# Kernel optimization log

Measured on AMD Instinct MI355X. Metric: run time of the kernel, lower is better.

## Reference

```python
import jax, jax.numpy as jnp
import numpy as np
import math

B, Q, D = 2, 2048, 1024
H, R = 16, 12
DH = D // H
RHO = 2.0
MAX_OFFSET = 6.0


def setup_inputs() -> dict:
    key = jax.random.key(0)
    ks = jax.random.split(key, 16)
    s = 0.02
    inp = {
        'x': jax.random.normal(ks[0], (B, Q, D), dtype=jnp.float32),
        'wq': jax.random.normal(ks[1], (D, D), dtype=jnp.float32) * s,
        'bq': jnp.zeros((D,), jnp.float32),
        'wk': jax.random.normal(ks[2], (D, D), dtype=jnp.float32) * s,
        'bk': jnp.zeros((D,), jnp.float32),
        'wv': jax.random.normal(ks[3], (D, D), dtype=jnp.float32) * s,
        'bv': jnp.zeros((D,), jnp.float32),
        'wo': jax.random.normal(ks[4], (D, D), dtype=jnp.float32) * s,
        'bo': jnp.zeros((D,), jnp.float32),
        'dw_w': jax.random.normal(ks[5], (D, 1, 3), dtype=jnp.float32) * s,  # depthwise conv1d k=3
        'dw_b': jnp.zeros((D,), jnp.float32),
        'pw_w': jax.random.normal(ks[6], (H * R, D), dtype=jnp.float32) * s,  # pointwise conv1d k=1
        'pw_b': jnp.zeros((H * R,), jnp.float32),
        'rel_scale': jnp.asarray(0.1, jnp.float32),
    }
    return inp


def _split_heads(y):
    b, q, d = y.shape
    return y.reshape(b, q, H, DH).transpose(0, 2, 1, 3)  # (b,h,q,dh)


def _sample(seq, pos):
    # seq: (b,h,q,dh), pos: (b,h,q,r) fractional positions -> (b,h,q,r,dh)
    b, h, q, dh = seq.shape
    low = jnp.clip(jnp.floor(pos), 0, q - 1).astype(jnp.int32)
    high = jnp.clip(jnp.ceil(pos), 0, q - 1).astype(jnp.int32)
    frac = (pos - low.astype(pos.dtype))[..., None]
    bi = jnp.arange(b)[:, None, None, None]
    hi = jnp.arange(h)[None, :, None, None]
    gl = seq[bi, hi, low]   # (b,h,q,r,dh) gather
    gh = seq[bi, hi, high]
    return gl * (1.0 - frac) + gh * frac


def reference(x, wq, bq, wk, bk, wv, bv, wo, bo, dw_w, dw_b, pw_w, pw_b, rel_scale):
    b, q, d = x.shape
    q_lin = x @ wq.T + bq
    qh = _split_heads(q_lin)
    kh = _split_heads(x @ wk.T + bk)
    vh = _split_heads(x @ wv.T + bv)

    # learned offsets: depthwise conv (k=3, groups=d) -> gelu -> pointwise conv
    feat = q_lin.transpose(0, 2, 1)  # (b,d,q)
    dw = jax.lax.conv_general_dilated(
        feat, dw_w, window_strides=(1,), padding=[(1, 1)],
        feature_group_count=D, dimension_numbers=('NCH', 'OIH', 'NCH'))
    dw = dw + dw_b[None, :, None]
    g = jax.nn.gelu(dw, approximate=False)
    off = jnp.einsum('od,bdq->boq', pw_w, g) + pw_b[None, :, None]  # (b,h*r,q)
    off = off.transpose(0, 2, 1).reshape(b, q, H, R).transpose(0, 2, 1, 3)  # (b,h,q,r)
    off = jnp.tanh(off) * MAX_OFFSET

    base = jnp.arange(q, dtype=x.dtype)[None, None, :, None]
    anchor = jnp.linspace(-RHO, RHO, R, dtype=x.dtype)[None, None, None, :]
    positions = jnp.clip(base + anchor + off, 0.0, q - 1.0)  # (b,h,q,r)

    sk = _sample(kh, positions)  # (b,h,q,r,dh)
    sv = _sample(vh, positions)

    scores = jnp.einsum('bhqd,bhqrd->bhqr', qh, sk) / math.sqrt(DH)
    rel = positions - jnp.arange(q, dtype=x.dtype)[None, None, :, None]
    scores = scores - rel_scale * jnp.abs(rel)
    attn = jax.nn.softmax(scores, axis=-1)
    out = jnp.einsum('bhqr,bhqrd->bhqd', attn, sv)  # (b,h,q,dh)
    out = out.transpose(0, 2, 1, 3).reshape(b, q, d)
    return out @ wo.T + bo
```

## Files before the change

### kernel.cpp

```cpp
#include <hip/hip_runtime.h>
#include <math.h>

constexpr int B_  = 2;
constexpr int Q_  = 2048;
constexpr int D_  = 1024;
constexpr int H_  = 16;
constexpr int R_  = 12;
constexpr int DH_ = 64;
constexpr int M_  = B_ * Q_;
constexpr int HR_ = H_ * R_;
constexpr int NQKV = 3 * D_;

typedef short bf16x8 __attribute__((ext_vector_type(8)));
typedef float f32x4  __attribute__((ext_vector_type(4)));

__device__ __forceinline__ float bf2f(unsigned short u) {
    return __uint_as_float(((unsigned)u) << 16);
}
__device__ __forceinline__ unsigned short f2bf(float f) {
    unsigned u = __float_as_uint(f);
    return (unsigned short)((u + 0x7fffu + ((u >> 16) & 1u)) >> 16);
}

__global__ __launch_bounds__(256) void cvt_all(const float* __restrict__ x,
                                               const float* __restrict__ wq,
                                               const float* __restrict__ wk,
                                               const float* __restrict__ wv,
                                               const float* __restrict__ wo,
                                               const float* __restrict__ pww,
                                               const float* __restrict__ bq,
                                               const float* __restrict__ bk,
                                               const float* __restrict__ bv,
                                               unsigned short* __restrict__ xb,
                                               unsigned short* __restrict__ wqkv,
                                               unsigned short* __restrict__ wob,
                                               unsigned short* __restrict__ pwwb,
                                               float* __restrict__ bqkv) {
    const int blk = blockIdx.x;
    if (blk >= 4192) {
        const int i = (blk - 4192) * 256 + threadIdx.x;
        bqkv[i] = i < D_ ? bq[i] : (i < 2 * D_ ? bk[i - D_] : bv[i - 2 * D_]);
        return;
    }
    const int i = blk * 256 + threadIdx.x;
    const float* src;
    unsigned short* dst;
    int rel;
    if (i < 524288)       { src = x;   dst = xb;                          rel = i; }
    else if (i < 655360)  { src = wq;  dst = wqkv;                        rel = i - 524288; }
    else if (i < 786432)  { src = wk;  dst = wqkv + (size_t)D_ * D_;      rel = i - 655360; }
    else if (i < 917504)  { src = wv;  dst = wqkv + (size_t)2 * D_ * D_;  rel = i - 786432; }
    else if (i < 1048576) { src = wo;  dst = wob;                         rel = i - 917504; }
    else                  { src = pww; dst = pwwb;                        rel = i - 1048576; }

    const float4 a = ((const float4*)src)[2 * rel];
    const float4 b = ((const float4*)src)[2 * rel + 1];
    uint4 o;
    o.x = (unsigned)f2bf(a.x) | ((unsigned)f2bf(a.y) << 16);
    o.y = (unsigned)f2bf(a.z) | ((unsigned)f2bf(a.w) << 16);
    o.z = (unsigned)f2bf(b.x) | ((unsigned)f2bf(b.y) << 16);
    o.w = (unsigned)f2bf(b.z) | ((unsigned)f2bf(b.w) << 16);
    ((uint4*)dst)[rel] = o;
}

template <int BN, bool OUT_BF16>
__global__ __launch_bounds__(256) void gemm_mfma(const unsigned short* __restrict__ A,
                                                 const unsigned short* __restrict__ W,
                                                 const float* __restrict__ bias,
                                                 void* __restrict__ Cv,
                                                 int M, int N, int K) {
    constexpr int BM  = 128, BK = 64;
    constexpr int FN  = BN / 32;
    constexpr int CHA = BM / 8;
    constexpr int CHB = BN / 8;
    __shared__ unsigned short As[BM * BK];
    __shared__ unsigned short Bs[BN * BK];

    const int tid  = threadIdx.x;
    const int w    = tid >> 6, lane = tid & 63;
    const int wm   = w >> 1,   wn   = w & 1;

    const int nbx = gridDim.x;
    const int nwg = nbx * gridDim.y;
    int flat = blockIdx.y * nbx + blockIdx.x;
    flat = (flat & 7) * (nwg >> 3) + (flat >> 3);
    const int bm = (flat / nbx) * BM;
    const int bn = (flat % nbx) * BN;

    const int srow  = lane >> 3;
    const int sslot = (lane & 7) ^ (srow & 7);
    const int fr = lane & 15;
    const int s  = lane >> 4;
    const int fx = fr & 7;

    f32x4 acc[4][FN];
    #pragma unroll
    for (int i = 0; i < 4; ++i)
        #pragma unroll
        for (int j = 0; j < FN; ++j) acc[i][j] = (f32x4){0.f, 0.f, 0.f, 0.f};

    for (int k0 = 0; k0 < K; k0 += BK) {
        __syncthreads();
        #pragma unroll
        for (int c = w; c < CHA; c += 4) {
            const unsigned short* g = A + (size_t)(bm + c * 8 + srow) * K + k0 + sslot * 8;
            __builtin_amdgcn_global_load_lds(
                (const __attribute__((address_space(1))) void*)g,
                (__attribute__((address_space(3))) void*)((char*)As + c * 1024), 16, 0, 0);
        }
        #pragma unroll
        for (int c = w; c < CHB; c += 4) {
            const unsigned short* g = W + (size_t)(bn + c * 8 + srow) * K + k0 + sslot * 8;
            __builtin_amdgcn_global_load_lds(
                (const __attribute__((address_space(1))) void*)g,
                (__attribute__((address_space(3))) void*)((char*)Bs + c * 1024), 16, 0, 0);
        }
        __syncthreads();

        #pragma unroll
        for (int ks = 0; ks < 2; ++ks) {
            const int sl = (((ks << 2) | s) ^ fx) * 8;
            bf16x8 af[4];
            #pragma unroll
            for (int i = 0; i < 4; ++i)
                af[i] = *(const bf16x8*)(As + (wm * 64 + i * 16 + fr) * BK + sl);
            #pragma unroll
            for (int j = 0; j < FN; ++j) {
                const bf16x8 bfrag = *(const bf16x8*)(Bs + (wn * (BN / 2) + j * 16 + fr) * BK + sl);
                #pragma unroll
                for (int i = 0; i < 4; ++i)
                    acc[i][j] = __builtin_amdgcn_mfma_f32_16x16x32_bf16(af[i], bfrag, acc[i][j], 0, 0, 0);
            }
        }
    }

    #pragma unroll
    for (int j = 0; j < FN; ++j) {
        const int col = bn + wn * (BN / 2) + j * 16 + fr;
        const float bv = bias[col];
        #pragma unroll
        for (int i = 0; i < 4; ++i) {
            const int row0 = bm + wm * 64 + i * 16 + ((lane >> 4) << 2);
            #pragma unroll
            for (int ii = 0; ii < 4; ++ii) {
                const float v = acc[i][j][ii] + bv;
                if constexpr (OUT_BF16)
                    ((unsigned short*)Cv)[(size_t)(row0 + ii) * N + col] = f2bf(v);
                else
                    ((float*)Cv)[(size_t)(row0 + ii) * N + col] = v;
            }
        }
    }
}

__global__ __launch_bounds__(256) void dwpw_kernel(const unsigned short* __restrict__ qkv,
                                                   const float* __restrict__ dww,
                                                   const float* __restrict__ dwb,
                                                   const unsigned short* __restrict__ pwwb,
                                                   const float* __restrict__ pwb,
                                                   unsigned short* __restrict__ offb) {
    __shared__ unsigned short As[16 * 1024];
    __shared__ unsigned short Bs[192 * 64];
    const int tid  = threadIdx.x;
    const int w    = tid >> 6, lane = tid & 63;
    const int m0   = blockIdx.x * 16;

    for (int u = tid; u < 16 * 128; u += 256) {
        const int r  = u >> 7;
        const int c8 = (u & 127) << 3;
        const int m  = m0 + r;
        const int t  = m & (Q_ - 1);
        const unsigned short* row = qkv + (size_t)m * NQKV + c8;

        unsigned short cur[8], prv[8] = {0}, nxt[8] = {0};
        *(uint4*)cur = *(const uint4*)row;
        if (t > 0)      *(uint4*)prv = *(const uint4*)(row - NQKV);
        if (t < Q_ - 1) *(uint4*)nxt = *(const uint4*)(row + NQKV);

        float dwl[24];
        #pragma unroll
        for (int q2 = 0; q2 < 6; ++q2)
            *(f32x4*)&dwl[q2 * 4] = *(const f32x4*)&dww[c8 * 3 + q2 * 4];
        float db[8];
        *(f32x4*)&db[0] = *(const f32x4*)&dwb[c8];
        *(f32x4*)&db[4] = *(const f32x4*)&dwb[c8 + 4];

        unsigned short o[8];
        #pragma unroll
        for (int j = 0; j < 8; ++j) {
            float v = bf2f(prv[j]) * dwl[j * 3 + 0] + bf2f(cur[j]) * dwl[j * 3 + 1]
                    + bf2f(nxt[j]) * dwl[j * 3 + 2] + db[j];
            v = 0.5f * v * (1.0f + erff(v * 0.70710678118654752f));
            o[j] = f2bf(v);
        }
        const int slot = (c8 >> 3) ^ (r & 7);
        *(uint4*)(As + r * 1024 + slot * 8) = *(uint4*)o;
    }
    __syncthreads();

    const int srow  = lane >> 3;
    const int sslot = (lane & 7) ^ (srow & 7);
    const int fr = lane & 15;
    const int s  = lane >> 4;
    const int fx = fr & 7;

    f32x4 acc[3];
    #pragma unroll
    for (int j = 0; j < 3; ++j) acc[j] = (f32x4){0.f, 0.f, 0.f, 0.f};

    for (int k0 = 0; k0 < 1024; k0 += 64) {
        if (k0) __syncthreads();
        #pragma unroll
        for (int c = w; c < 24; c += 4) {
            const unsigned short* g = pwwb + (size_t)(c * 8 + srow) * 1024 + k0 + sslot * 8;
            __builtin_amdgcn_global_load_lds(
                (const __attribute__((address_space(1))) void*)g,
                (__attribute__((address_space(3))) void*)((char*)Bs + c * 1024), 16, 0, 0);
        }
        __syncthreads();

        #pragma unroll
        for (int ks = 0; ks < 2; ++ks) {
            const int aslot = ((k0 >> 3) + ((ks << 2) | s)) ^ fx;
            const bf16x8 af = *(const bf16x8*)(As + fr * 1024 + aslot * 8);
            const int sl = (((ks << 2) | s) ^ fx) * 8;
            #pragma unroll
            for (int j = 0; j < 3; ++j) {
                const bf16x8 bfrag = *(const bf16x8*)(Bs + (w * 48 + j * 16 + fr) * 64 + sl);
                acc[j] = __builtin_amdgcn_mfma_f32_16x16x32_bf16(af, bfrag, acc[j], 0, 0, 0);
            }
        }
    }

    #pragma unroll
    for (int j = 0; j < 3; ++j) {
        const int n = w * 48 + j * 16 + fr;
        const float bv = pwb[n];
        const int row0 = (lane >> 4) << 2;
        #pragma unroll
        for (int ii = 0; ii < 4; ++ii)
            offb[(size_t)(m0 + row0 + ii) * HR_ + n] = f2bf(acc[j][ii] + bv);
    }
}

__global__ __launch_bounds__(256) void coeff_pv_kernel(const unsigned short* __restrict__ qkv,
                                                       const unsigned short* __restrict__ offb,
                                                       const float* __restrict__ rel_scale_p,
                                                       unsigned short* __restrict__ attb) {
    __shared__ __align__(16) float S[4][16][33];
    __shared__ __align__(16) float C[4][16][32];
    const int tid  = threadIdx.x;
    const int w    = tid >> 6, lane = tid & 63;
    const int tile = blockIdx.x * 4 + w;
    const int t0   = (tile & 127) << 4;
    const int h    = (tile >> 7) & 15;
    const int b    = tile >> 11;
    const int fr   = lane & 15;
    const int fo   = (lane >> 4) << 3;

    const unsigned short* qrow = qkv + (size_t)(b * Q_ + t0 + fr) * NQKV + h * DH_ + fo;
    const bf16x8 af0 = *(const bf16x8*)qrow;
    const bf16x8 af1 = *(const bf16x8*)(qrow + 32);

    f32x4 acc0 = (f32x4){0.f, 0.f, 0.f, 0.f};
    f32x4 acc1 = acc0;
    {
        int j = min(max(t0 - 8 + fr, 0), Q_ - 1);
        const unsigned short* krow = qkv + (size_t)(b * Q_ + j) * NQKV + D_ + h * DH_ + fo;
        acc0 = __builtin_amdgcn_mfma_f32_16x16x32_bf16(af0, *(const bf16x8*)krow, acc0, 0, 0, 0);
        acc0 = __builtin_amdgcn_mfma_f32_16x16x32_bf16(af1, *(const bf16x8*)(krow + 32), acc0, 0, 0, 0);
    }
    {
        int j = min(max(t0 + 8 + fr, 0), Q_ - 1);
        const unsigned short* krow = qkv + (size_t)(b * Q_ + j) * NQKV + D_ + h * DH_ + fo;
        acc1 = __builtin_amdgcn_mfma_f32_16x16x32_bf16(af0, *(const bf16x8*)krow, acc1, 0, 0, 0);
        acc1 = __builtin_amdgcn_mfma_f32_16x16x32_bf16(af1, *(const bf16x8*)(krow + 32), acc1, 0, 0, 0);
    }

    float vj[32];
    {
        const unsigned short* vb = qkv + (size_t)b * Q_ * NQKV + 2 * D_ + h * DH_ + lane;
        #pragma unroll
        for (int i2 = 0; i2 < 32; ++i2) {
            const int j = min(max(t0 - 8 + i2, 0), Q_ - 1);
            vj[i2] = bf2f(vb[(size_t)j * NQKV]);
        }
    }

    const int row0 = (lane >> 4) << 2;
    #pragma unroll
    for (int ii = 0; ii < 4; ++ii) {
        S[w][row0 + ii][fr]      = acc0[ii];
        S[w][row0 + ii][16 + fr] = acc1[ii];
    }
    {
        const int tr = lane >> 2, cg = (lane & 3) << 3;
        #pragma unroll
        for (int k = 0; k < 8; ++k) C[w][tr][cg + k] = 0.f;
    }
    __syncthreads();

    const int tloc = lane & 15;
    const int rs   = lane >> 4;
    const int t    = t0 + tloc;
    const float rel_scale = rel_scale_p[0];
    const unsigned short* offrow = offb + (size_t)(b * Q_ + t) * HR_ + h * R_;

    float sc[3], fr3[3];
    int   cl[3], ch[3];
    #pragma unroll
    for (int i = 0; i < 3; ++i) {
        const int r = rs * 3 + i;
        const float off    = bf2f(offrow[r]);
        const float anchor = -2.0f + (4.0f / 11.0f) * (float)r;
        float pos = (float)t + anchor + 6.0f * tanhf(off);
        pos = fminf(fmaxf(pos, 0.0f), (float)(Q_ - 1));
        const float fl = floorf(pos);
        const int lo = (int)fl;
        const int hi = (int)ceilf(pos);
        const float f = pos - fl;
        cl[i] = lo - t0 + 8;
        ch[i] = hi - t0 + 8;
        fr3[i] = f;
        const float slo = S[w][tloc][cl[i]];
        const float shi = S[w][tloc][ch[i]];
        sc[i] = (slo * (1.0f - f) + shi * f) * 0.125f - rel_scale * fabsf(pos - (float)t);
    }

    float mx = fmaxf(fmaxf(sc[0], sc[1]), sc[2]);
    mx = fmaxf(mx, __shfl_xor(mx, 16));
    mx = fmaxf(mx, __shfl_xor(mx, 32));
    float e[3];
    #pragma unroll
    for (int i = 0; i < 3; ++i) e[i] = expf(sc[i] - mx);
    float sum = e[0] + e[1] + e[2];
    sum += __shfl_xor(sum, 16);
    sum += __shfl_xor(sum, 32);
    const float inv = 1.0f / sum;

    #pragma unroll
    for (int i = 0; i < 3; ++i) {
        const float wgt = e[i] * inv;
        atomicAdd(&C[w][tloc][cl[i]], wgt * (1.0f - fr3[i]));
        atomicAdd(&C[w][tloc][ch[i]], wgt * fr3[i]);
    }
    __syncthreads();

    #pragma unroll
    for (int tl = 0; tl < 16; ++tl) {
        const int st = tl & ~3;
        float cw[20];
        #pragma unroll
        for (int q2 = 0; q2 < 5; ++q2)
            *(f32x4*)&cw[q2 * 4] = *(const f32x4*)&C[w][tl][st + q2 * 4];
        float acc2 = 0.f;
        #pragma unroll
        for (int k = 0; k <= 16; ++k)
            acc2 = fmaf(cw[tl - st + k], vj[tl + k], acc2);
        attb[(size_t)(b * Q_ + t0 + tl) * D_ + h * DH_ + lane] = f2bf(acc2);
    }
}

extern "C" void kernel_launch(void* const* d_in, const int* in_sizes, int n_in,
                              void* d_out, int out_size, void* d_ws, size_t ws_size,
                              hipStream_t stream) {
    const float* x    = (const float*)d_in[0];
    const float* wq   = (const float*)d_in[1];
    const float* bq   = (const float*)d_in[2];
    const float* wk   = (const float*)d_in[3];
    const float* bk   = (const float*)d_in[4];
    const float* wv   = (const float*)d_in[5];
    const float* bv   = (const float*)d_in[6];
    const float* wo   = (const float*)d_in[7];
    const float* bo   = (const float*)d_in[8];
    const float* dww  = (const float*)d_in[9];
    const float* dwb  = (const float*)d_in[10];
    const float* pww  = (const float*)d_in[11];
    const float* pwb  = (const float*)d_in[12];
    const float* rsc  = (const float*)d_in[13];
    float* out = (float*)d_out;

    unsigned short* xb   = (unsigned short*)d_ws;
    unsigned short* wqkv = xb   + (size_t)M_ * D_;
    unsigned short* wob  = wqkv + (size_t)NQKV * D_;
    unsigned short* pwwb = wob  + (size_t)D_ * D_;
    unsigned short* qkv  = pwwb + (size_t)HR_ * D_;
    unsigned short* offb = qkv  + (size_t)M_ * NQKV;
    unsigned short* attb = offb + (size_t)M_ * HR_;
    float*          bqkv = (float*)(attb + (size_t)M_ * D_);

    dim3 blk(256);

    hipLaunchKernelGGL(cvt_all, dim3(4204), blk, 0, stream,
                       x, wq, wk, wv, wo, pww, bq, bk, bv, xb, wqkv, wob, pwwb, bqkv);

    hipLaunchKernelGGL((gemm_mfma<128, true>), dim3(NQKV / 128, M_ / 128), blk, 0, stream,
                       xb, wqkv, bqkv, qkv, M_, NQKV, D_);

    hipLaunchKernelGGL(dwpw_kernel, dim3(M_ / 16), blk, 0, stream,
                       qkv, dww, dwb, pwwb, pwb, offb);

    hipLaunchKernelGGL(coeff_pv_kernel, dim3(B_ * H_ * (Q_ / 16) / 4), blk, 0, stream,
                       qkv, offb, rsc, attb);

    hipLaunchKernelGGL((gemm_mfma<128, false>), dim3(D_ / 128, M_ / 128), blk, 0, stream,
                       attb, wob, bo, out, M_, D_, D_);
}
```

Baseline: 101.7 us.

## Add 256x256 eight-phase pipelined QKV GEMM with direct-to-LDS loads

Replaces the QKV projection GEMM with a dedicated 512-thread kernel using 256x256 tiles, double-buffered LDS filled via global_load_lds, XOR-swizzled LDS reads, and an eight-phase interleave of loads and MFMA with setprio, plus XCD-aware block remapping. The aim is to hide global memory latency behind MFMA work and raise arithmetic intensity per block. It also shrinks the output-projection GEMM tile to BN=64 to launch more blocks. The cost is 128KB of LDS per block, hard-coded shapes, and a hand-tuned waitcnt schedule that is easy to get wrong.

```diff
diff --git a/kernel.cpp b/kernel.cpp
--- a/kernel.cpp
+++ b/kernel.cpp
@@ -63,6 +63,124 @@
     ((uint4*)dst)[rel] = o;
 }
 
+#define REG_(par, op, half) ((par)*32768 + (op)*16384 + (half)*8192)
+
+#define STAGE8(op, half, par, tile)                                            \
+  if ((tile) < 16) {                                                           \
+    const unsigned short* g_ = ((op) ? Wp : Ap) +                              \
+        (size_t)((half)*128 + w*16 + srow) * 1024 + (tile)*64 + sslot*8;       \
+    unsigned short* l_ = (unsigned short*)lds + REG_(par,op,half) + w*1024;    \
+    __builtin_amdgcn_global_load_lds(                                          \
+        (const __attribute__((address_space(1))) void*)g_,                     \
+        (__attribute__((address_space(3))) void*)l_, 16, 0, 0);                \
+    __builtin_amdgcn_global_load_lds(                                          \
+        (const __attribute__((address_space(1))) void*)(g_ + 8 * 1024),        \
+        (__attribute__((address_space(3))) void*)(l_ + 512), 16, 0, 0);        \
+  }
+
+#define LDA8(par, mf, kc) \
+  (*(const bf16x8*)&lds[REG_(par,0,wr) + ((mf)*16 + fr)*64 + ((((kc)*4 + s) ^ (fr & 7))*8)])
+#define LDB8(par, nf, kc) \
+  (*(const bf16x8*)&lds[REG_(par,1,(wc>>1)) + ((wc&1)*64 + (nf)*16 + fr)*64 + ((((kc)*4 + s) ^ (fr & 7))*8)])
+
+#define MFMA_PHASE(MB, BF, NOFS)                                               \
+  __builtin_amdgcn_s_barrier();                                                \
+  asm volatile("s_waitcnt lgkmcnt(0)" ::: "memory");                           \
+  __builtin_amdgcn_sched_barrier(0);                                           \
+  __builtin_amdgcn_s_setprio(1);                                               \
+  _Pragma("unroll") for (int kc = 0; kc < 2; ++kc)                             \
+    _Pragma("unroll") for (int nf = 0; nf < 2; ++nf)                           \
+      _Pragma("unroll") for (int mf = 0; mf < 4; ++mf)                         \
+        acc[(MB)+mf][(NOFS)+nf] = __builtin_amdgcn_mfma_f32_16x16x32_bf16(     \
+            af[mf][kc], BF[nf][kc], acc[(MB)+mf][(NOFS)+nf], 0, 0, 0);         \
+  __builtin_amdgcn_s_setprio(0);                                               \
+  __builtin_amdgcn_s_barrier();
+
+__global__ __launch_bounds__(512, 2) void gemm_qkv_8ph(
+    const unsigned short* __restrict__ A,
+    const unsigned short* __restrict__ W,
+    const float* __restrict__ bias,
+    unsigned short* __restrict__ C) {
+    __shared__ unsigned short lds[65536];
+    const int tid  = threadIdx.x;
+    const int w    = tid >> 6, lane = tid & 63;
+    const int wr   = w >> 2,   wc   = w & 3;
+    int flat = blockIdx.x;
+    flat = (flat & 7) * 24 + (flat >> 3);
+    const int bm = (flat / 12) * 256;
+    const int bn = (flat % 12) * 256;
+    const int fr = lane & 15, s = lane >> 4;
+    const int srow  = lane >> 3;
+    const int sslot = (lane & 7) ^ srow;
+    const unsigned short* Ap = A + (size_t)bm * 1024;
+    const unsigned short* Wp = W + (size_t)bn * 1024;
+
+    f32x4 acc[8][4];
+    #pragma unroll
+    for (int i = 0; i < 8; ++i)
+        #pragma unroll
+        for (int j = 0; j < 4; ++j) acc[i][j] = (f32x4){0.f, 0.f, 0.f, 0.f};
+
+    bf16x8 af[4][2], bfA[2][2], bfB[2][2];
+
+    STAGE8(1, 0, 0, 0) STAGE8(1, 1, 0, 0) STAGE8(0, 0, 0, 0) STAGE8(0, 1, 0, 0)
+    STAGE8(1, 0, 1, 1) STAGE8(0, 0, 1, 1)
+    asm volatile("s_waitcnt vmcnt(4)" ::: "memory");
+    __builtin_amdgcn_s_barrier();
+
+    for (int j = 0; j < 8; ++j) {
+        const int T = 2 * j;
+        #pragma unroll
+        for (int mf = 0; mf < 4; ++mf) { af[mf][0] = LDA8(0, mf, 0); af[mf][1] = LDA8(0, mf, 1); }
+        #pragma unroll
+        for (int nf = 0; nf < 2; ++nf) { bfA[nf][0] = LDB8(0, nf, 0); bfA[nf][1] = LDB8(0, nf, 1); }
+        STAGE8(1, 1, 1, T + 1)
+        MFMA_PHASE(0, bfA, 0)
+        #pragma unroll
+        for (int nf = 0; nf < 2; ++nf) { bfB[nf][0] = LDB8(0, nf + 2, 0); bfB[nf][1] = LDB8(0, nf + 2, 1); }
+        STAGE8(0, 1, 1, T + 1)
+        MFMA_PHASE(0, bfB, 2)
+        #pragma unroll
+        for (int mf = 0; mf < 4; ++mf) { af[mf][0] = LDA8(0, mf + 4, 0); af[mf][1] = LDA8(0, mf + 4, 1); }
+        STAGE8(1, 0, 0, T + 2)
+        MFMA_PHASE(4, bfA, 0)
+        STAGE8(1, 1, 0, T + 2)
+        if (j < 7) { asm volatile("s_waitcnt vmcnt(4)" ::: "memory"); }
+        else       { asm volatile("s_waitcnt vmcnt(0)" ::: "memory"); }
+        MFMA_PHASE(4, bfB, 2)
+        #pragma unroll
+        for (int mf = 0; mf < 4; ++mf) { af[mf][0] = LDA8(1, mf, 0); af[mf][1] = LDA8(1, mf, 1); }
+        #pragma unroll
+        for (int nf = 0; nf < 2; ++nf) { bfA[nf][0] = LDB8(1, nf, 0); bfA[nf][1] = LDB8(1, nf, 1); }
+        STAGE8(0, 0, 0, T + 2)
+        MFMA_PHASE(0, bfA, 0)
+        #pragma unroll
+        for (int nf = 0; nf < 2; ++nf) { bfB[nf][0] = LDB8(1, nf + 2, 0); bfB[nf][1] = LDB8(1, nf + 2, 1); }
+        STAGE8(0, 1, 0, T + 2)
+        MFMA_PHASE(0, bfB, 2)
+        #pragma unroll
+        for (int mf = 0; mf < 4; ++mf) { af[mf][0] = LDA8(1, mf + 4, 0); af[mf][1] = LDA8(1, mf + 4, 1); }
+        STAGE8(1, 0, 1, T + 3)
+        MFMA_PHASE(4, bfA, 0)
+        STAGE8(0, 0, 1, T + 3)
+        asm volatile("s_waitcnt vmcnt(4)" ::: "memory");
+        MFMA_PHASE(4, bfB, 2)
+    }
+
+    #pragma unroll
+    for (int nf = 0; nf < 4; ++nf) {
+        const int col = bn + wc * 64 + nf * 16 + fr;
+        const float bv = bias[col];
+        #pragma unroll
+        for (int mf = 0; mf < 8; ++mf) {
+            const int row0 = bm + wr * 128 + mf * 16 + s * 4;
+            #pragma unroll
+            for (int ii = 0; ii < 4; ++ii)
+                C[(size_t)(row0 + ii) * NQKV + col] = f2bf(acc[mf][nf][ii] + bv);
+        }
+    }
+}
+
 template <int BN, bool OUT_BF16>
 __global__ __launch_bounds__(256) void gemm_mfma(const unsigned short* __restrict__ A,
                                                  const unsigned short* __restrict__ W,
@@ -394,8 +512,8 @@
     hipLaunchKernelGGL(cvt_all, dim3(4204), blk, 0, stream,
                        x, wq, wk, wv, wo, pww, bq, bk, bv, xb, wqkv, wob, pwwb, bqkv);
 
-    hipLaunchKernelGGL((gemm_mfma<128, true>), dim3(NQKV / 128, M_ / 128), blk, 0, stream,
-                       xb, wqkv, bqkv, qkv, M_, NQKV, D_);
+    hipLaunchKernelGGL(gemm_qkv_8ph, dim3(192), dim3(512), 0, stream,
+                       xb, wqkv, bqkv, qkv);
 
     hipLaunchKernelGGL(dwpw_kernel, dim3(M_ / 16), blk, 0, stream,
                        qkv, dww, dwb, pwwb, pwb, offb);
@@ -403,6 +521,6 @@
     hipLaunchKernelGGL(coeff_pv_kernel, dim3(B_ * H_ * (Q_ / 16) / 4), blk, 0, stream,
                        qkv, offb, rsc, attb);
 
-    hipLaunchKernelGGL((gemm_mfma<128, false>), dim3(D_ / 128, M_ / 128), blk, 0, stream,
+    hipLaunchKernelGGL((gemm_mfma<64, false>), dim3(D_ / 64, M_ / 128), blk, 0, stream,
                        attb, wob, bo, out, M_, D_, D_);
 }
```

Result: no change. 103.1 us (+1.4%).
